# Kernel optimization log

Measured on AMD Instinct MI355X. Metric: run time of the kernel, lower is better.

The kernel has to match this reference:

```python
import math
import jax, jax.numpy as jnp
import numpy as np

ANCHOR_AREAS = [4 * 4, 16 * 16, 64 * 64, 128 * 128]
ASPECT_RATIOS = [1 / 2.0, 1 / 1.0, 2 / 1.0]
SCALE_RATIOS = [1.0, 2.0, 3 / 4.0]
NUM_ANCHORS = len(ASPECT_RATIOS) * len(SCALE_RATIOS)  # 9


def _anchor_wh():
    wh = []
    for s in ANCHOR_AREAS:
        for ar in ASPECT_RATIOS:
            h = math.sqrt(s / ar)
            w = ar * h
            for sr in SCALE_RATIOS:
                wh.append([w * sr, h * sr])
    return np.asarray(wh, np.float32).reshape(len(ANCHOR_AREAS), NUM_ANCHORS, 2)


def build_anchor_boxes(input_size):
    """All anchors in (cx, cy, w, h), shape [A, 4]. Static numpy computation."""
    wh = _anchor_wh()
    out = []
    for i in range(len(ANCHOR_AREAS)):
        fm = int(math.ceil(input_size / 2.0 ** (i + 2)))
        grid = input_size / fm
        centers = (np.arange(fm, dtype=np.float32) + 0.5) * grid
        gx, gy = np.meshgrid(centers, centers)  # gx varies along width
        xy = np.stack([gx, gy], axis=-1)  # [fm, fm, 2]
        xy = np.broadcast_to(xy[:, :, None, :], (fm, fm, NUM_ANCHORS, 2))
        whl = np.broadcast_to(wh[i][None, None, :, :], (fm, fm, NUM_ANCHORS, 2))
        out.append(np.concatenate([xy, whl], axis=-1).reshape(-1, 4))
    return jnp.asarray(np.concatenate(out, 0), jnp.float32)


def box_iou_xywh(anchors, boxes):
    """anchors [A,4] xywh, boxes [B,N,4] xywh -> IoU [B,A,N] (kuangliu +1 convention)."""
    a1 = jnp.concatenate([anchors[:, :2] - anchors[:, 2:] / 2,
                          anchors[:, :2] + anchors[:, 2:] / 2], axis=-1)  # [A,4]
    b1 = jnp.concatenate([boxes[..., :2] - boxes[..., 2:] / 2,
                          boxes[..., :2] + boxes[..., 2:] / 2], axis=-1)  # [B,N,4]
    lt = jnp.maximum(a1[None, :, None, :2], b1[:, None, :, :2])  # [B,A,N,2]
    rb = jnp.minimum(a1[None, :, None, 2:], b1[:, None, :, 2:])
    wh = jnp.clip(rb - lt + 1.0, 0.0)
    inter = wh[..., 0] * wh[..., 1]  # [B,A,N]
    area_a = (a1[:, 2] - a1[:, 0] + 1.0) * (a1[:, 3] - a1[:, 1] + 1.0)  # [A]
    area_b = (b1[..., 2] - b1[..., 0] + 1.0) * (b1[..., 3] - b1[..., 1] + 1.0)  # [B,N]
    return inter / (area_a[None, :, None] + area_b[:, None, :] - inter)


def setup_inputs() -> dict:
    key = jax.random.key(0)
    k1, k2, k3 = jax.random.split(key, 3)
    B, N, S = 4, 64, 512
    # valid xyxy boxes inside the image
    x1y1 = jax.random.uniform(k1, (B, N, 2), jnp.float32, 0.0, S - 130.0)
    wh = jax.random.uniform(k2, (B, N, 2), jnp.float32, 4.0, 128.0)
    boxes = jnp.concatenate([x1y1, x1y1 + wh], axis=-1)
    labels = jax.random.randint(k3, (B, N), 0, 10, jnp.int64 if jax.config.jax_enable_x64 else jnp.int32)
    return {"labels": labels, "boxes": boxes, "input_size": S}


def reference(labels, boxes, input_size):
    B = boxes.shape[0]
    anchors = build_anchor_boxes(int(input_size))  # [A,4] xywh
    # xyxy -> xywh (kuangliu: center (a+b)/2, size b-a+1)
    a, b = boxes[..., :2], boxes[..., 2:]
    boxes_xywh = jnp.concatenate([(a + b) / 2.0, b - a + 1.0], axis=-1)  # [B,N,4]
    ious = box_iou_xywh(anchors, boxes_xywh)  # [B,A,N]
    max_ious = jnp.max(ious, axis=2)  # [B,A]
    max_ids = jnp.argmax(ious, axis=2)  # [B,A]
    gather = jax.vmap(lambda t, i: t[i])
    matched = gather(boxes_xywh, max_ids)  # [B,A,4]
    loc_xy = (matched[..., :2] - anchors[None, :, :2]) / anchors[None, :, 2:]
    loc_wh = jnp.log(matched[..., 2:] / anchors[None, :, 2:])
    loc_targets = jnp.concatenate([loc_xy, loc_wh], axis=-1)  # [B,A,4]
    cls = gather(labels, max_ids)  # [B,A]
    cls = jnp.where(max_ious < 0.5, 0, cls)
    cls = jnp.where((max_ious > 0.4) & (max_ious < 0.5), -1, cls)
    return cls, loc_targets
```

## Files before the change

kernel.cpp:

```cpp
#include <hip/hip_runtime.h>
#include <math.h>


__global__ __launch_bounds__(256) void anchors_kernel(
    const int*   __restrict__ labels,
    const float* __restrict__ boxes,
    float*       __restrict__ out,
    int B, int N, int A, int S)
{
    __shared__ float4 s_corn[256];
    __shared__ float  s_area[256];
    __shared__ float4 s_xywh[256];
    __shared__ int    s_lab[256];

    const int t    = threadIdx.x;
    const int lane = t & 63;
    const int wid  = t >> 6;
    const int b    = blockIdx.y;

    const int wr0 = blockIdx.x * 256 + wid * 64;
    if (wr0 >= A) return;

    int r0 = wr0;
    int lvl = 0, fm = S >> 2;
    #pragma unroll
    for (int i = 0; i < 3; ++i) {
        int cnt = fm * fm * 9;
        if (r0 >= cnt) { r0 -= cnt; lvl = i + 1; fm >>= 1; }
    }
    const int   lfm  = 31 - __clz(fm);
    const float grid = (float)(4 << lvl);
    const float sl   = (float)((lvl == 3) ? 128 : (4 << (2 * lvl)));

    const int cell_lo = r0 / 9;
    const int cell_hi = (r0 + 63) / 9;
    const int ci_lo = cell_lo >> lfm, ci_hi = cell_hi >> lfm;
    int cj_lo, cj_hi;
    if (ci_lo == ci_hi) { cj_lo = cell_lo & (fm - 1); cj_hi = cell_hi & (fm - 1); }
    else                { cj_lo = 0;                  cj_hi = fm - 1; }
    const float ext  = 1.41422f * sl + 2.0f;
    const float bbx1 = ((float)cj_lo + 0.5f) * grid - ext;
    const float bbx2 = ((float)cj_hi + 0.5f) * grid + ext;
    const float bby1 = ((float)ci_lo + 0.5f) * grid - ext;
    const float bby2 = ((float)ci_hi + 0.5f) * grid + ext;

    int L;
    {
        bool  pred = false;
        float cx = 0, cy = 0, w = 0, h = 0, bx1 = 0, by1 = 0, bx2 = 0, by2 = 0;
        int   lab = 0;
        if (lane < N) {
            float4 bx = reinterpret_cast<const float4*>(boxes)[b * N + lane];
            pred = (fminf(bbx2, bx.z) - fmaxf(bbx1, bx.x) + 1.0f > 0.0f) &&
                   (fminf(bby2, bx.w) - fmaxf(bby1, bx.y) + 1.0f > 0.0f);
            pred = pred || (lane == 0);
            cx = (bx.x + bx.z) * 0.5f;
            cy = (bx.y + bx.w) * 0.5f;
            w  = bx.z - bx.x + 1.0f;
            h  = bx.w - bx.y + 1.0f;
            bx1 = cx - w * 0.5f;  by1 = cy - h * 0.5f;
            bx2 = cx + w * 0.5f;  by2 = cy + h * 0.5f;
            lab = labels[b * N + lane];
        }
        unsigned long long mask = __ballot(pred);
        if (pred) {
            int pos = wid * 64 + __popcll(mask & ((1ull << lane) - 1ull));
            s_corn[pos] = make_float4(bx1, by1, bx2, by2);
            s_area[pos] = (bx2 - bx1 + 1.0f) * (by2 - by1 + 1.0f);
            s_xywh[pos] = make_float4(cx, cy, w, h);
            s_lab[pos]  = lab;
        }
        L = __popcll(mask);
    }

    const int r    = r0 + lane;
    const int cell = r / 9;
    const int k    = r - cell * 9;
    const int cj   = cell & (fm - 1);
    const int ci   = cell >> lfm;

    const float cwk =
        (k < 3) ? ((k == 0) ? 0.70710678118654752f
                 : (k == 1) ? 1.41421356237309515f
                            : 0.53033008588991064f)
      : (k < 6) ? ((k == 3) ? 1.0f : (k == 4) ? 2.0f : 0.75f)
                : ((k == 6) ? 1.41421356237309515f
                 : (k == 7) ? 2.82842712474619029f
                            : 1.06066017177982129f);
    const float chk =
        (k < 3) ? ((k == 0) ? 1.41421356237309515f
                 : (k == 1) ? 2.82842712474619029f
                            : 1.06066017177982129f)
      : (k < 6) ? ((k == 3) ? 1.0f : (k == 4) ? 2.0f : 0.75f)
                : ((k == 6) ? 0.70710678118654752f
                 : (k == 7) ? 1.41421356237309515f
                            : 0.53033008588991064f);
    const float aw = cwk * sl;
    const float ah = chk * sl;

    const float acx = ((float)cj + 0.5f) * grid;
    const float acy = ((float)ci + 0.5f) * grid;
    const float ax1 = acx - aw * 0.5f;
    const float ay1 = acy - ah * 0.5f;
    const float ax2 = acx + aw * 0.5f;
    const float ay2 = acy + ah * 0.5f;
    const float area_a = (ax2 - ax1 + 1.0f) * (ay2 - ay1 + 1.0f);

    float best_in = 0.0f, best_un = 1.0f;
    int   bj = 0;
    const int base = wid * 64;
    for (int j = 0; j < L; ++j) {
        float4 c = s_corn[base + j];
        float iw = fmaxf(fminf(ax2, c.z) - fmaxf(ax1, c.x) + 1.0f, 0.0f);
        float ih = fmaxf(fminf(ay2, c.w) - fmaxf(ay1, c.y) + 1.0f, 0.0f);
        float in_ = iw * ih;
        float un_ = (area_a + s_area[base + j]) - in_;
        bool better = (in_ * best_un) > (best_in * un_);
        best_in = better ? in_ : best_in;
        best_un = better ? un_ : best_un;
        bj      = better ? j   : bj;
    }
    float best;
    float4 m;
    int lab;
    if (best_in > 0.0f || true) {
        best = best_in / best_un;
        m    = s_xywh[base + bj];
        lab  = s_lab[base + bj];
    }

    int cls = lab;
    if (best < 0.5f) cls = 0;
    if (best > 0.4f && best < 0.5f) cls = -1;

    const float rcp_aw = __builtin_amdgcn_rcpf(aw);
    const float rcp_ah = __builtin_amdgcn_rcpf(ah);
    float4 loc;
    loc.x = (m.x - acx) * rcp_aw;
    loc.y = (m.y - acy) * rcp_ah;
    loc.z = __logf(m.z * rcp_aw);
    loc.w = __logf(m.w * rcp_ah);

    const size_t gid = (size_t)b * A + (size_t)(wr0 + lane);
    out[gid] = (float)cls;
    reinterpret_cast<float4*>(out + (size_t)B * A)[gid] = loc;
}

extern "C" void kernel_launch(void* const* d_in, const int* in_sizes, int n_in,
                              void* d_out, int out_size, void* d_ws, size_t ws_size,
                              hipStream_t stream) {
    const int S = 512;
    int A = 0;
    for (int i = 0; i < 4; ++i) {
        int f = (S + (1 << (i + 2)) - 1) >> (i + 2);
        A += f * f * 9;
    }
    const int B = out_size / (5 * A);
    const int N = in_sizes[0] / B;

    dim3 gridDim((A + 255) / 256, B);

    anchors_kernel<<<gridDim, 256, 0, stream>>>(
        (const int*)d_in[0], (const float*)d_in[1], (float*)d_out, B, N, A, S);
}
```

Before: 17.72 us.

## Replace LDS box compaction with register readlane iteration over ballot mask

```diff
diff --git a/kernel.cpp b/kernel.cpp
--- a/kernel.cpp
+++ b/kernel.cpp
@@ -8,14 +8,9 @@
     float*       __restrict__ out,
     int B, int N, int A, int S)
 {
-    __shared__ float4 s_corn[256];
-    __shared__ float  s_area[256];
-    __shared__ float4 s_xywh[256];
-    __shared__ int    s_lab[256];
-
     const int t    = threadIdx.x;
     const int lane = t & 63;
-    const int wid  = t >> 6;
+    const int wid  = __builtin_amdgcn_readfirstlane(t >> 6);
     const int b    = blockIdx.y;
 
     const int wr0 = blockIdx.x * 256 + wid * 64;
@@ -44,34 +39,25 @@
     const float bby1 = ((float)ci_lo + 0.5f) * grid - ext;
     const float bby2 = ((float)ci_hi + 0.5f) * grid + ext;
 
-    int L;
-    {
-        bool  pred = false;
-        float cx = 0, cy = 0, w = 0, h = 0, bx1 = 0, by1 = 0, bx2 = 0, by2 = 0;
-        int   lab = 0;
-        if (lane < N) {
-            float4 bx = reinterpret_cast<const float4*>(boxes)[b * N + lane];
-            pred = (fminf(bbx2, bx.z) - fmaxf(bbx1, bx.x) + 1.0f > 0.0f) &&
-                   (fminf(bby2, bx.w) - fmaxf(bby1, bx.y) + 1.0f > 0.0f);
-            pred = pred || (lane == 0);
-            cx = (bx.x + bx.z) * 0.5f;
-            cy = (bx.y + bx.w) * 0.5f;
-            w  = bx.z - bx.x + 1.0f;
-            h  = bx.w - bx.y + 1.0f;
-            bx1 = cx - w * 0.5f;  by1 = cy - h * 0.5f;
-            bx2 = cx + w * 0.5f;  by2 = cy + h * 0.5f;
-            lab = labels[b * N + lane];
-        }
-        unsigned long long mask = __ballot(pred);
-        if (pred) {
-            int pos = wid * 64 + __popcll(mask & ((1ull << lane) - 1ull));
-            s_corn[pos] = make_float4(bx1, by1, bx2, by2);
-            s_area[pos] = (bx2 - bx1 + 1.0f) * (by2 - by1 + 1.0f);
-            s_xywh[pos] = make_float4(cx, cy, w, h);
-            s_lab[pos]  = lab;
-        }
-        L = __popcll(mask);
+    float bcx = 0, bcy = 0, bw = 0, bh = 0;
+    float kx1 = 0, ky1 = 0, kx2 = 0, ky2 = 0, karea = 0;
+    int   blab = 0;
+    bool  pred = false;
+    if (lane < N) {
+        float4 bx = reinterpret_cast<const float4*>(boxes)[b * N + lane];
+        pred = (fminf(bbx2, bx.z) - fmaxf(bbx1, bx.x) + 1.0f > 0.0f) &&
+               (fminf(bby2, bx.w) - fmaxf(bby1, bx.y) + 1.0f > 0.0f);
+        bcx = (bx.x + bx.z) * 0.5f;
+        bcy = (bx.y + bx.w) * 0.5f;
+        bw  = bx.z - bx.x + 1.0f;
+        bh  = bx.w - bx.y + 1.0f;
+        kx1 = bcx - bw * 0.5f;  ky1 = bcy - bh * 0.5f;
+        kx2 = bcx + bw * 0.5f;  ky2 = bcy + bh * 0.5f;
+        karea = (kx2 - kx1 + 1.0f) * (ky2 - ky1 + 1.0f);
+        blab  = labels[b * N + lane];
     }
+    unsigned long long mask = __ballot(pred);
+    mask |= 1ull;
 
     const int r    = r0 + lane;
     const int cell = r / 9;
@@ -108,26 +94,31 @@
 
     float best_in = 0.0f, best_un = 1.0f;
     int   bj = 0;
-    const int base = wid * 64;
-    for (int j = 0; j < L; ++j) {
-        float4 c = s_corn[base + j];
-        float iw = fmaxf(fminf(ax2, c.z) - fmaxf(ax1, c.x) + 1.0f, 0.0f);
-        float ih = fmaxf(fminf(ay2, c.w) - fmaxf(ay1, c.y) + 1.0f, 0.0f);
+    unsigned long long mm = mask;
+    while (mm) {
+        const int j = (int)__builtin_ctzll(mm);
+        mm &= mm - 1ull;
+        const float cbx1 = __int_as_float(__builtin_amdgcn_readlane(__float_as_int(kx1), j));
+        const float cby1 = __int_as_float(__builtin_amdgcn_readlane(__float_as_int(ky1), j));
+        const float cbx2 = __int_as_float(__builtin_amdgcn_readlane(__float_as_int(kx2), j));
+        const float cby2 = __int_as_float(__builtin_amdgcn_readlane(__float_as_int(ky2), j));
+        const float car  = __int_as_float(__builtin_amdgcn_readlane(__float_as_int(karea), j));
+        float iw = fmaxf(fminf(ax2, cbx2) - fmaxf(ax1, cbx1) + 1.0f, 0.0f);
+        float ih = fmaxf(fminf(ay2, cby2) - fmaxf(ay1, cby1) + 1.0f, 0.0f);
         float in_ = iw * ih;
-        float un_ = (area_a + s_area[base + j]) - in_;
+        float un_ = (area_a + car) - in_;
         bool better = (in_ * best_un) > (best_in * un_);
         best_in = better ? in_ : best_in;
         best_un = better ? un_ : best_un;
         bj      = better ? j   : bj;
     }
-    float best;
-    float4 m;
-    int lab;
-    if (best_in > 0.0f || true) {
-        best = best_in / best_un;
-        m    = s_xywh[base + bj];
-        lab  = s_lab[base + bj];
-    }
+    const float best = best_in / best_un;
+
+    const float mcx = __shfl(bcx, bj);
+    const float mcy = __shfl(bcy, bj);
+    const float mw  = __shfl(bw,  bj);
+    const float mh  = __shfl(bh,  bj);
+    const int   lab = __shfl(blab, bj);
 
     int cls = lab;
     if (best < 0.5f) cls = 0;
@@ -136,10 +127,10 @@
     const float rcp_aw = __builtin_amdgcn_rcpf(aw);
     const float rcp_ah = __builtin_amdgcn_rcpf(ah);
     float4 loc;
-    loc.x = (m.x - acx) * rcp_aw;
-    loc.y = (m.y - acy) * rcp_ah;
-    loc.z = __logf(m.z * rcp_aw);
-    loc.w = __logf(m.w * rcp_ah);
+    loc.x = (mcx - acx) * rcp_aw;
+    loc.y = (mcy - acy) * rcp_ah;
+    loc.z = __logf(mw * rcp_aw);
+    loc.w = __logf(mh * rcp_ah);
 
     const size_t gid = (size_t)b * A + (size_t)(wr0 + lane);
     out[gid] = (float)cls;
```

Result: slower. 20.17 us (+13.8%).
